# Optimization experiments

Measured on AMD Instinct MI355X. Metric: run time of the kernel, lower is better.

The kernel has to match this reference:

```python
import jax, jax.numpy as jnp
import numpy as np

NUM_LABELS = 1024
NUM_CAMS = 8


def setup_inputs() -> dict:
    key = jax.random.key(0)
    k1, k2, k3 = jax.random.split(key, 3)
    feats = jax.random.normal(k1, (16384, 2048), dtype=jnp.float32)
    labels = jax.random.randint(k2, (16384,), 0, NUM_LABELS, dtype=jnp.int64)
    cam_ids = jax.random.randint(k3, (16384,), 0, NUM_CAMS, dtype=jnp.int64)
    return {"feats": feats, "labels": labels, "cam_ids": cam_ids}


def reference(feats, labels, cam_ids):
    # Combined (person-id, camera-id) segment id -> fused segment-mean.
    seg = labels * NUM_CAMS + cam_ids  # [N]
    num_segments = NUM_LABELS * NUM_CAMS
    sums = jax.ops.segment_sum(feats, seg, num_segments=num_segments)  # [S, D]
    counts = jax.ops.segment_sum(jnp.ones_like(seg, dtype=feats.dtype), seg,
                                 num_segments=num_segments)  # [S]
    means = sums / jnp.maximum(counts, 1.0)[:, None]
    # targets[i] = mean of feats over group(label_i, cam_i); detached in torch.
    targets = jax.lax.stop_gradient(means[seg])  # [N, D]
    # SmoothL1 (beta=1), reduction='mean'
    d = feats - targets
    ad = jnp.abs(d)
    loss = jnp.mean(jnp.where(ad < 1.0, 0.5 * d * d, ad - 0.5))
    return loss
```

## Files before the change

### kernel.cpp

```cpp
#include <hip/hip_runtime.h>
#include <hip/hip_bf16.h>

#define N_ROWS 16384
#define D_COLS 2048
#define NUM_LABELS 1024
#define NUM_CAMS 8
#define NUM_SEG (NUM_LABELS * NUM_CAMS)
#define MAXPER 64
#define R_REG 8
#define INFO_INTS 16
#define INFO_IDX 12
#define F4_PER_ROW (D_COLS / 4)
#define NUM_BLOCKS (NUM_SEG * 2)

__global__ void build_lists_kernel(const int* __restrict__ labels,
                                   const int* __restrict__ cams,
                                   int* __restrict__ counts,
                                   int* __restrict__ lists) {
    int i = blockIdx.x * blockDim.x + threadIdx.x;
    if (i < N_ROWS) {
        int seg = labels[i] * NUM_CAMS + cams[i];
        int pos = atomicAdd(&counts[seg], 1);
        if (pos < MAXPER) lists[seg * MAXPER + pos] = i;
    }
}

__global__ __launch_bounds__(256) void repack_kernel(const int* __restrict__ counts,
                                                     const int* __restrict__ lists,
                                                     int* __restrict__ seginfo) {
    int seg = blockIdx.x * blockDim.x + threadIdx.x;
    if (seg < NUM_SEG) {
        int cnt = counts[seg];
        int c = cnt < INFO_IDX ? cnt : INFO_IDX;
        int* o = seginfo + seg * INFO_INTS;
        o[0] = cnt;
#pragma unroll
        for (int r = 0; r < INFO_IDX; ++r)
            o[1 + r] = (r < c) ? lists[seg * MAXPER + r] : 0;
    }
}

__device__ __forceinline__ float smooth_l1(float d) {
    float ad = fabsf(d);
    return ad < 1.0f ? 0.5f * d * d : ad - 0.5f;
}

__global__ __launch_bounds__(256, 8) void seg_loss_kernel(const float* __restrict__ feats,
                                                          const int* __restrict__ seginfo,
                                                          const int* __restrict__ lists,
                                                          float* __restrict__ partials) {
    int bid  = blockIdx.x;
    int seg  = bid >> 1;
    int half = bid & 1;
    int tid  = threadIdx.x;

    const int* info = seginfo + seg * INFO_INTS;
    int cnt  = info[0];
    int rows = cnt < R_REG ? cnt : R_REG;

    const float4* base = (const float4*)feats + (half * 256 + tid);

    float4 v[R_REG];
#pragma unroll
    for (int r = 0; r < R_REG; ++r) {
        v[r] = make_float4(0.f, 0.f, 0.f, 0.f);
        if (r < rows)
            v[r] = base[(size_t)info[1 + r] * F4_PER_ROW];
    }

    float mx = 0.f, my = 0.f, mz = 0.f, mw = 0.f;
#pragma unroll
    for (int r = 0; r < R_REG; ++r) {
        mx += v[r].x; my += v[r].y; mz += v[r].z; mw += v[r].w;
    }

    if (cnt > R_REG) {
        for (int r = R_REG; r < cnt && r < INFO_IDX; ++r) {
            float4 a = base[(size_t)info[1 + r] * F4_PER_ROW];
            mx += a.x; my += a.y; mz += a.z; mw += a.w;
        }
        for (int r = INFO_IDX; r < cnt && r < MAXPER; ++r) {
            float4 a = base[(size_t)lists[seg * MAXPER + r] * F4_PER_ROW];
            mx += a.x; my += a.y; mz += a.z; mw += a.w;
        }
    }

    float inv = 1.0f / (float)(cnt > 0 ? cnt : 1);
    mx *= inv; my *= inv; mz *= inv; mw *= inv;

    float loss = 0.0f;
#pragma unroll
    for (int r = 0; r < R_REG; ++r) {
        float w = (r < rows) ? 1.0f : 0.0f;
        loss += w * (smooth_l1(v[r].x - mx) + smooth_l1(v[r].y - my)
                   + smooth_l1(v[r].z - mz) + smooth_l1(v[r].w - mw));
    }
    if (cnt > R_REG) {
        for (int r = R_REG; r < cnt && r < INFO_IDX; ++r) {
            float4 a = base[(size_t)info[1 + r] * F4_PER_ROW];
            loss += smooth_l1(a.x - mx) + smooth_l1(a.y - my)
                  + smooth_l1(a.z - mz) + smooth_l1(a.w - mw);
        }
        for (int r = INFO_IDX; r < cnt && r < MAXPER; ++r) {
            float4 a = base[(size_t)lists[seg * MAXPER + r] * F4_PER_ROW];
            loss += smooth_l1(a.x - mx) + smooth_l1(a.y - my)
                  + smooth_l1(a.z - mz) + smooth_l1(a.w - mw);
        }
    }

    for (int o = 32; o > 0; o >>= 1)
        loss += __shfl_down(loss, o, 64);

    __shared__ float wsum[4];
    int lane = tid & 63;
    int wid  = tid >> 6;
    if (lane == 0) wsum[wid] = loss;
    __syncthreads();
    if (tid == 0)
        partials[bid] = wsum[0] + wsum[1] + wsum[2] + wsum[3];
}

__global__ __launch_bounds__(256) void reduce_kernel(const float* __restrict__ partials,
                                                     float* __restrict__ out) {
    int tid = threadIdx.x;
    float s = 0.0f;
    for (int i = tid; i < NUM_BLOCKS; i += 256)
        s += partials[i];

    for (int o = 32; o > 0; o >>= 1)
        s += __shfl_down(s, o, 64);

    __shared__ float wsum[4];
    int lane = tid & 63;
    int wid  = tid >> 6;
    if (lane == 0) wsum[wid] = s;
    __syncthreads();
    if (tid == 0)
        out[0] = (wsum[0] + wsum[1] + wsum[2] + wsum[3])
               * (1.0f / ((float)N_ROWS * (float)D_COLS));
}

extern "C" void kernel_launch(void* const* d_in, const int* in_sizes, int n_in,
                              void* d_out, int out_size, void* d_ws, size_t ws_size,
                              hipStream_t stream) {
    const float* feats = (const float*)d_in[0];
    const int* labels  = (const int*)d_in[1];
    const int* cams    = (const int*)d_in[2];
    float* out = (float*)d_out;

    int* counts     = (int*)d_ws;
    int* lists      = counts + NUM_SEG;
    int* seginfo    = lists + NUM_SEG * MAXPER;
    float* partials = (float*)(seginfo + NUM_SEG * INFO_INTS);

    hipMemsetAsync(counts, 0, NUM_SEG * sizeof(int), stream);

    build_lists_kernel<<<(N_ROWS + 255) / 256, 256, 0, stream>>>(labels, cams, counts, lists);
    repack_kernel<<<(NUM_SEG + 255) / 256, 256, 0, stream>>>(counts, lists, seginfo);
    seg_loss_kernel<<<NUM_BLOCKS, 256, 0, stream>>>(feats, seginfo, lists, partials);
    reduce_kernel<<<1, 256, 0, stream>>>(partials, out);
}
```

Baseline: 220.9 us.

## Process eight segments per block with double-buffered software-pipelined row loads

Each block now handles a group of eight segments instead of one, so the grid shrinks eightfold. While one segment's mean and loss are computed, the next segment's first four rows are already being loaded. The unconditional fast-path loads rely on padding empty slots with the segment's first row index. This cuts launch and block overhead and hides gather latency, at the cost of less parallelism per block and extra redundant loads for small segments.

```diff
diff --git a/kernel.cpp b/kernel.cpp
--- a/kernel.cpp
+++ b/kernel.cpp
@@ -7,11 +7,11 @@
 #define NUM_CAMS 8
 #define NUM_SEG (NUM_LABELS * NUM_CAMS)
 #define MAXPER 64
-#define R_REG 8
-#define INFO_INTS 16
-#define INFO_IDX 12
+#define GSEG 8
+#define NUM_BLOCKS (NUM_SEG / GSEG * 2)
+#define FAST_R 4
+#define INFO_INTS 8
 #define F4_PER_ROW (D_COLS / 4)
-#define NUM_BLOCKS (NUM_SEG * 2)
 
 __global__ void build_lists_kernel(const int* __restrict__ labels,
                                    const int* __restrict__ cams,
@@ -31,12 +31,14 @@
     int seg = blockIdx.x * blockDim.x + threadIdx.x;
     if (seg < NUM_SEG) {
         int cnt = counts[seg];
-        int c = cnt < INFO_IDX ? cnt : INFO_IDX;
+        int c = cnt < FAST_R ? cnt : FAST_R;
+        int first = (cnt > 0) ? lists[seg * MAXPER] : 0;
         int* o = seginfo + seg * INFO_INTS;
         o[0] = cnt;
 #pragma unroll
-        for (int r = 0; r < INFO_IDX; ++r)
-            o[1 + r] = (r < c) ? lists[seg * MAXPER + r] : 0;
+        for (int r = 0; r < FAST_R; ++r)
+            o[1 + r] = (r < c) ? lists[seg * MAXPER + r] : first;
+        o[5] = 0; o[6] = 0; o[7] = 0;
     }
 }
 
@@ -45,67 +47,72 @@
     return ad < 1.0f ? 0.5f * d * d : ad - 0.5f;
 }
 
-__global__ __launch_bounds__(256, 8) void seg_loss_kernel(const float* __restrict__ feats,
-                                                          const int* __restrict__ seginfo,
-                                                          const int* __restrict__ lists,
-                                                          float* __restrict__ partials) {
+__global__ __launch_bounds__(256, 8) void group_loss_kernel(const float* __restrict__ feats,
+                                                            const int* __restrict__ seginfo,
+                                                            const int* __restrict__ lists,
+                                                            float* __restrict__ partials) {
     int bid  = blockIdx.x;
-    int seg  = bid >> 1;
+    int grp  = bid >> 1;
     int half = bid & 1;
     int tid  = threadIdx.x;
+    int seg0 = grp * GSEG;
 
-    const int* info = seginfo + seg * INFO_INTS;
-    int cnt  = info[0];
-    int rows = cnt < R_REG ? cnt : R_REG;
+    const int* info = seginfo + (size_t)grp * GSEG * INFO_INTS;
+    const float4* base = (const float4*)feats + (half * 256 + tid);
+    float loss = 0.0f;
 
-    const float4* base = (const float4*)feats + (half * 256 + tid);
+    auto load4 = [&](float4* v, int s, int& cnt) {
+        const int* rec = info + s * INFO_INTS;
+        cnt = rec[0];
+#pragma unroll
+        for (int r = 0; r < FAST_R; ++r)
+            v[r] = base[(size_t)rec[1 + r] * F4_PER_ROW];
+    };
 
-    float4 v[R_REG];
+    auto consume = [&](const float4* v, int s, int cnt) {
+        float mx = 0.f, my = 0.f, mz = 0.f, mw = 0.f;
 #pragma unroll
-    for (int r = 0; r < R_REG; ++r) {
-        v[r] = make_float4(0.f, 0.f, 0.f, 0.f);
-        if (r < rows)
-            v[r] = base[(size_t)info[1 + r] * F4_PER_ROW];
-    }
+        for (int r = 0; r < FAST_R; ++r) {
+            float w = (r < cnt) ? 1.0f : 0.0f;
+            mx = fmaf(w, v[r].x, mx);
+            my = fmaf(w, v[r].y, my);
+            mz = fmaf(w, v[r].z, mz);
+            mw = fmaf(w, v[r].w, mw);
+        }
+        if (cnt > FAST_R) {
+            for (int r = FAST_R; r < cnt && r < MAXPER; ++r) {
+                float4 a = base[(size_t)lists[(seg0 + s) * MAXPER + r] * F4_PER_ROW];
+                mx += a.x; my += a.y; mz += a.z; mw += a.w;
+            }
+        }
+        float inv = 1.0f / (float)(cnt > 0 ? cnt : 1);
+        mx *= inv; my *= inv; mz *= inv; mw *= inv;
 
-    float mx = 0.f, my = 0.f, mz = 0.f, mw = 0.f;
 #pragma unroll
-    for (int r = 0; r < R_REG; ++r) {
-        mx += v[r].x; my += v[r].y; mz += v[r].z; mw += v[r].w;
-    }
+        for (int r = 0; r < FAST_R; ++r) {
+            float w = (r < cnt) ? 1.0f : 0.0f;
+            loss += w * (smooth_l1(v[r].x - mx) + smooth_l1(v[r].y - my)
+                       + smooth_l1(v[r].z - mz) + smooth_l1(v[r].w - mw));
+        }
+        if (cnt > FAST_R) {
+            for (int r = FAST_R; r < cnt && r < MAXPER; ++r) {
+                float4 a = base[(size_t)lists[(seg0 + s) * MAXPER + r] * F4_PER_ROW];
+                loss += smooth_l1(a.x - mx) + smooth_l1(a.y - my)
+                      + smooth_l1(a.z - mz) + smooth_l1(a.w - mw);
+            }
+        }
+    };
 
-    if (cnt > R_REG) {
-        for (int r = R_REG; r < cnt && r < INFO_IDX; ++r) {
-            float4 a = base[(size_t)info[1 + r] * F4_PER_ROW];
-            mx += a.x; my += a.y; mz += a.z; mw += a.w;
-        }
-        for (int r = INFO_IDX; r < cnt && r < MAXPER; ++r) {
-            float4 a = base[(size_t)lists[seg * MAXPER + r] * F4_PER_ROW];
-            mx += a.x; my += a.y; mz += a.z; mw += a.w;
-        }
-    }
-
-    float inv = 1.0f / (float)(cnt > 0 ? cnt : 1);
-    mx *= inv; my *= inv; mz *= inv; mw *= inv;
-
-    float loss = 0.0f;
-#pragma unroll
-    for (int r = 0; r < R_REG; ++r) {
-        float w = (r < rows) ? 1.0f : 0.0f;
-        loss += w * (smooth_l1(v[r].x - mx) + smooth_l1(v[r].y - my)
-                   + smooth_l1(v[r].z - mz) + smooth_l1(v[r].w - mw));
-    }
-    if (cnt > R_REG) {
-        for (int r = R_REG; r < cnt && r < INFO_IDX; ++r) {
-            float4 a = base[(size_t)info[1 + r] * F4_PER_ROW];
-            loss += smooth_l1(a.x - mx) + smooth_l1(a.y - my)
-                  + smooth_l1(a.z - mz) + smooth_l1(a.w - mw);
-        }
-        for (int r = INFO_IDX; r < cnt && r < MAXPER; ++r) {
-            float4 a = base[(size_t)lists[seg * MAXPER + r] * F4_PER_ROW];
-            loss += smooth_l1(a.x - mx) + smooth_l1(a.y - my)
-                  + smooth_l1(a.z - mz) + smooth_l1(a.w - mw);
-        }
+    float4 va[FAST_R], vb[FAST_R];
+    int ca, cb;
+    load4(va, 0, ca);
+#pragma unroll 1
+    for (int s = 0; s < GSEG; s += 2) {
+        load4(vb, s + 1, cb);
+        consume(va, s, ca);
+        if (s + 2 < GSEG)
+            load4(va, s + 2, ca);
+        consume(vb, s + 1, cb);
     }
 
     for (int o = 32; o > 0; o >>= 1)
@@ -157,6 +164,6 @@
 
     build_lists_kernel<<<(N_ROWS + 255) / 256, 256, 0, stream>>>(labels, cams, counts, lists);
     repack_kernel<<<(NUM_SEG + 255) / 256, 256, 0, stream>>>(counts, lists, seginfo);
-    seg_loss_kernel<<<NUM_BLOCKS, 256, 0, stream>>>(feats, seginfo, lists, partials);
+    group_loss_kernel<<<NUM_BLOCKS, 256, 0, stream>>>(feats, seginfo, lists, partials);
     reduce_kernel<<<1, 256, 0, stream>>>(partials, out);
 }
```

Measured after the change: 208.3 us. -5.7%, faster.
